# Kernel tuning notes

Hardware: AMD Instinct MI355X
Metric: run time of the kernel (lower is better)

The kernel has to match this reference:

```python
import jax, jax.numpy as jnp
import numpy as np
import math

B, S, D, H = 4, 2048, 1024, 16
DH = D // H  # per-head dim = 64
MASK_VAL = -1000000.0


def setup_inputs() -> dict:
    key = jax.random.key(0)
    ks = jax.random.split(key, 9)
    queries = jax.random.normal(ks[0], (B, S, D), dtype=jnp.float32)
    keys = jax.random.normal(ks[1], (B, S, D), dtype=jnp.float32)
    values = jax.random.normal(ks[2], (B, S, D), dtype=jnp.float32)
    valid_lens = jax.random.randint(ks[3], (B,), 0, S, dtype=jnp.int32)
    scale = 1.0 / math.sqrt(D)
    Wq = jax.random.normal(ks[4], (D, D), dtype=jnp.float32) * scale
    Wk = jax.random.normal(ks[5], (D, D), dtype=jnp.float32) * scale
    Wv = jax.random.normal(ks[6], (D, D), dtype=jnp.float32) * scale
    Wo = jax.random.normal(ks[7], (D, D), dtype=jnp.float32) * scale
    return {"queries": queries, "keys": keys, "values": values,
            "valid_lens": valid_lens, "Wq": Wq, "Wk": Wk, "Wv": Wv, "Wo": Wo}


def _split_heads(x):  # [B,S,D] -> [B,H,S,DH]
    b, s, _ = x.shape
    return x.reshape(b, s, H, DH).transpose(0, 2, 1, 3)


def reference(queries, keys, values, valid_lens, Wq, Wk, Wv, Wo):
    q = _split_heads(queries @ Wq)  # [B,H,S,DH]
    k = _split_heads(keys @ Wk)
    v = _split_heads(values @ Wv)
    scores = jnp.einsum('bhqd,bhkd->bhqk', q, k) / jnp.sqrt(jnp.float32(DH))
    # mask key positions >= valid_len[b] (sequence_mask with value=-1e6)
    key_pos = jnp.arange(S)  # [S]
    mask = key_pos[None, None, None, :] < valid_lens[:, None, None, None]  # [B,1,1,S]
    scores = jnp.where(mask, scores, MASK_VAL)
    attn = jax.nn.softmax(scores, axis=-1)  # [B,H,S,S] -- the 1GB intermediate
    out = jnp.einsum('bhqk,bhkd->bhqd', attn, v)  # [B,H,S,DH]
    out = out.transpose(0, 2, 1, 3).reshape(B, S, D)  # concat heads
    return out @ Wo
```

## Files before the change

### kernel.cpp

```cpp
#include <hip/hip_runtime.h>

#define BB 4
#define SS 2048
#define DD 1024
#define HH 16
#define DHH 64

typedef _Float16 half8 __attribute__((ext_vector_type(8)));
typedef _Float16 half4v __attribute__((ext_vector_type(4)));
typedef float floatx4 __attribute__((ext_vector_type(4)));

#define GLOBAL_AS __attribute__((address_space(1)))
#define LDS_AS __attribute__((address_space(3)))

__global__ void prep_kernel(const float* __restrict__ q, const float* __restrict__ k,
                            const float* __restrict__ v, const float* __restrict__ wq,
                            const float* __restrict__ wk, const float* __restrict__ wv,
                            const float* __restrict__ wo, _Float16* __restrict__ wt,
                            _Float16* __restrict__ acat, float* __restrict__ dout) {
  int bx = blockIdx.x;
  if (bx < 4096) {
    __shared__ float tile[32][33];
    int z = bx >> 10, rem = bx & 1023;
    const float* w = (z == 0) ? wq : (z == 1) ? wk : (z == 2) ? wv : wo;
    float scale = (z == 0) ? 0.125f : 1.0f;
    _Float16* dst = wt + (size_t)z * 1048576;
    int k0 = (rem >> 5) * 32, n0 = (rem & 31) * 32;
    int tx = threadIdx.x & 31, ty = threadIdx.x >> 5;
#pragma unroll
    for (int r = ty; r < 32; r += 8) tile[r][tx] = w[(size_t)(k0 + r) * 1024 + n0 + tx];
    __syncthreads();
#pragma unroll
    for (int r = ty; r < 32; r += 8)
      dst[(size_t)(n0 + r) * 1024 + k0 + tx] = (_Float16)(tile[tx][r] * scale);
  } else if (bx < 16384) {
    int idx = bx - 4096;
    int z = idx >> 12, xx = idx & 4095;
    const float* src = (z == 0) ? q : (z == 1) ? k : v;
    size_t i = ((size_t)xx * 256 + threadIdx.x) * 8;
    float4 f0 = *(const float4*)(src + i);
    float4 f1 = *(const float4*)(src + i + 4);
    half8 h = {(_Float16)f0.x, (_Float16)f0.y, (_Float16)f0.z, (_Float16)f0.w,
               (_Float16)f1.x, (_Float16)f1.y, (_Float16)f1.z, (_Float16)f1.w};
    *(half8*)(acat + (size_t)z * 8388608 + i) = h;
  } else {
    int idx = bx - 16384;
    size_t i = ((size_t)idx * 256 + threadIdx.x) * 8;
    float4 zz = {0.f, 0.f, 0.f, 0.f};
    *(float4*)(dout + i) = zz;
    *(float4*)(dout + i + 4) = zz;
  }
}

__global__ __launch_bounds__(256) void qkv_gemm(const _Float16* __restrict__ Acat,
                                                const _Float16* __restrict__ Wt,
                                                _Float16* __restrict__ Qf,
                                                _Float16* __restrict__ Kf,
                                                _Float16* __restrict__ Vt) {
  __shared__ _Float16 lA[128 * 32];
  __shared__ _Float16 lB[128 * 32];
  int tid = threadIdx.x;
  int wave = tid >> 6, lane = tid & 63, quad = lane >> 4, l15 = lane & 15;
  int bn = blockIdx.x, bm = blockIdx.y;
  int proj = bm >> 6;
  int wm = wave >> 1, wn = wave & 1;

  const _Float16* A = Acat + (size_t)bm * 128 * 1024;
  const _Float16* W = Wt + (size_t)proj * 1024 * 1024;

  floatx4 fzero = {0.f, 0.f, 0.f, 0.f};
  floatx4 acc[4][4];
#pragma unroll
  for (int i = 0; i < 4; ++i)
#pragma unroll
    for (int j = 0; j < 4; ++j) acc[i][j] = fzero;

  int g0 = tid, g1 = 256 + tid;
  int row0 = g0 >> 2, gc0 = (g0 & 3) ^ ((row0 >> 1) & 3);
  int row1 = g1 >> 2, gc1 = (g1 & 3) ^ ((row1 >> 1) & 3);
  const _Float16* a0 = A + ((size_t)row0 * 1024 + gc0 * 8);
  const _Float16* a1 = A + ((size_t)row1 * 1024 + gc1 * 8);
  const _Float16* b0 = W + ((size_t)(bn * 128 + row0) * 1024 + gc0 * 8);
  const _Float16* b1 = W + ((size_t)(bn * 128 + row1) * 1024 + gc1 * 8);

  for (int k0 = 0; k0 < 1024; k0 += 32) {
    __builtin_amdgcn_global_load_lds((const GLOBAL_AS void*)(a0 + k0),
                                     (LDS_AS void*)(lA + g0 * 8), 16, 0, 0);
    __builtin_amdgcn_global_load_lds((const GLOBAL_AS void*)(a1 + k0),
                                     (LDS_AS void*)(lA + g1 * 8), 16, 0, 0);
    __builtin_amdgcn_global_load_lds((const GLOBAL_AS void*)(b0 + k0),
                                     (LDS_AS void*)(lB + g0 * 8), 16, 0, 0);
    __builtin_amdgcn_global_load_lds((const GLOBAL_AS void*)(b1 + k0),
                                     (LDS_AS void*)(lB + g1 * 8), 16, 0, 0);
    __syncthreads();

    half8 af[4], bf[4];
#pragma unroll
    for (int i = 0; i < 4; ++i) {
      int row = wm * 64 + i * 16 + l15;
      af[i] = *(const half8*)(lA + (row * 4 + (quad ^ ((row >> 1) & 3))) * 8);
    }
#pragma unroll
    for (int j = 0; j < 4; ++j) {
      int row = wn * 64 + j * 16 + l15;
      bf[j] = *(const half8*)(lB + (row * 4 + (quad ^ ((row >> 1) & 3))) * 8);
    }
#pragma unroll
    for (int i = 0; i < 4; ++i)
#pragma unroll
      for (int j = 0; j < 4; ++j)
        acc[i][j] = __builtin_amdgcn_mfma_f32_16x16x32_f16(af[i], bf[j], acc[i][j], 0, 0, 0);
    __syncthreads();
  }

  int rloc = (bm & 63) * 128;
#pragma unroll
  for (int i = 0; i < 4; ++i) {
#pragma unroll
    for (int j = 0; j < 4; ++j) {
      int rowb = rloc + wm * 64 + i * 16 + quad * 4;
      int col = bn * 128 + wn * 64 + j * 16 + l15;
      if (proj < 2) {
        _Float16* dst = (proj == 0) ? Qf : Kf;
#pragma unroll
        for (int r = 0; r < 4; ++r)
          dst[(size_t)(rowb + r) * 1024 + col] = (_Float16)acc[i][j][r];
      } else {
        int b = rowb >> 11, s = rowb & 2047;
        half4v pk = {(_Float16)acc[i][j][0], (_Float16)acc[i][j][1],
                     (_Float16)acc[i][j][2], (_Float16)acc[i][j][3]};
        *(half4v*)(Vt + (size_t)(b * 1024 + col) * 2048 + s) = pk;
      }
    }
  }
}

__global__ __launch_bounds__(256) void gemm_out(const _Float16* __restrict__ A,
                                                const _Float16* __restrict__ Wt,
                                                float* __restrict__ C) {
  __shared__ _Float16 lA[128 * 32];
  __shared__ _Float16 lB[128 * 32];
  int tid = threadIdx.x;
  int wave = tid >> 6, lane = tid & 63, quad = lane >> 4, l15 = lane & 15;
  int bn = blockIdx.x, bm = blockIdx.y, kz = blockIdx.z;
  int wm = wave >> 1, wn = wave & 1;

  floatx4 fzero = {0.f, 0.f, 0.f, 0.f};
  floatx4 acc[4][4];
#pragma unroll
  for (int i = 0; i < 4; ++i)
#pragma unroll
    for (int j = 0; j < 4; ++j) acc[i][j] = fzero;

  int g0 = tid, g1 = 256 + tid;
  int row0 = g0 >> 2, gc0 = (g0 & 3) ^ ((row0 >> 1) & 3);
  int row1 = g1 >> 2, gc1 = (g1 & 3) ^ ((row1 >> 1) & 3);
  const _Float16* a0 = A + ((size_t)(bm * 128 + row0) * 1024 + gc0 * 8);
  const _Float16* a1 = A + ((size_t)(bm * 128 + row1) * 1024 + gc1 * 8);
  const _Float16* b0 = Wt + ((size_t)(bn * 128 + row0) * 1024 + gc0 * 8);
  const _Float16* b1 = Wt + ((size_t)(bn * 128 + row1) * 1024 + gc1 * 8);

  int kbeg = kz * 512, kend = kbeg + 512;
  for (int k0 = kbeg; k0 < kend; k0 += 32) {
    __builtin_amdgcn_global_load_lds((const GLOBAL_AS void*)(a0 + k0),
                                     (LDS_AS void*)(lA + g0 * 8), 16, 0, 0);
    __builtin_amdgcn_global_load_lds((const GLOBAL_AS void*)(a1 + k0),
                                     (LDS_AS void*)(lA + g1 * 8), 16, 0, 0);
    __builtin_amdgcn_global_load_lds((const GLOBAL_AS void*)(b0 + k0),
                                     (LDS_AS void*)(lB + g0 * 8), 16, 0, 0);
    __builtin_amdgcn_global_load_lds((const GLOBAL_AS void*)(b1 + k0),
                                     (LDS_AS void*)(lB + g1 * 8), 16, 0, 0);
    __syncthreads();

    half8 af[4], bf[4];
#pragma unroll
    for (int i = 0; i < 4; ++i) {
      int row = wm * 64 + i * 16 + l15;
      af[i] = *(const half8*)(lA + (row * 4 + (quad ^ ((row >> 1) & 3))) * 8);
    }
#pragma unroll
    for (int j = 0; j < 4; ++j) {
      int row = wn * 64 + j * 16 + l15;
      bf[j] = *(const half8*)(lB + (row * 4 + (quad ^ ((row >> 1) & 3))) * 8);
    }
#pragma unroll
    for (int i = 0; i < 4; ++i)
#pragma unroll
      for (int j = 0; j < 4; ++j)
        acc[i][j] = __builtin_amdgcn_mfma_f32_16x16x32_f16(af[i], bf[j], acc[i][j], 0, 0, 0);
    __syncthreads();
  }

#pragma unroll
  for (int i = 0; i < 4; ++i)
#pragma unroll
    for (int j = 0; j < 4; ++j) {
      int rowb = bm * 128 + wm * 64 + i * 16 + quad * 4;
      int col = bn * 128 + wn * 64 + j * 16 + l15;
#pragma unroll
      for (int r = 0; r < 4; ++r)
        atomicAdd(&C[(size_t)(rowb + r) * 1024 + col], acc[i][j][r]);
    }
}

__global__ __launch_bounds__(256) void attn_kernel(const _Float16* __restrict__ Q,
                                                   const _Float16* __restrict__ K,
                                                   const _Float16* __restrict__ Vt,
                                                   const int* __restrict__ vlens,
                                                   _Float16* __restrict__ O) {
  __shared__ _Float16 lK[64 * 64];
  __shared__ _Float16 lV[64 * 64];
  __shared__ _Float16 lP[4 * 16 * 64];

  int tid = threadIdx.x, wave = tid >> 6, lane = tid & 63, quad = lane >> 4, l15 = lane & 15;
  int bh = blockIdx.y, b = bh >> 4, h = bh & 15;
  int q0 = blockIdx.x * 64;
  int vlen = vlens[b];
  int nch = (vlen == 0) ? (SS / 64) : ((vlen + 63) >> 6);
  float mask_val = (vlen == 0) ? 0.0f : -1.0e6f;

  const _Float16* qb = Q + ((size_t)(b * SS + q0 + wave * 16 + l15) * DD + h * 64 + quad * 8);
  half8 qf0 = *(const half8*)qb;
  half8 qf1 = *(const half8*)(qb + 32);

  float l_part[4] = {0.f, 0.f, 0.f, 0.f};
  floatx4 fzero = {0.f, 0.f, 0.f, 0.f};
  floatx4 o[4];
#pragma unroll
  for (int j = 0; j < 4; ++j) o[j] = fzero;

  for (int kc = 0; kc < nch; ++kc) {
    int kb = kc * 64;
#pragma unroll
    for (int ss = tid; ss < 512; ss += 256) {
      int row = ss >> 3, gc = ss & 7;
      int sidx = (row * 8 + (gc ^ (row & 7))) * 8;
      *(half8*)(lK + sidx) =
          *(const half8*)(K + ((size_t)(b * SS + kb + row) * DD + h * 64 + gc * 8));
      *(half8*)(lV + sidx) =
          *(const half8*)(Vt + ((size_t)(b * DD + h * 64 + row) * SS + kb + gc * 8));
    }
    __syncthreads();

    floatx4 sacc[4];
#pragma unroll
    for (int j = 0; j < 4; ++j) sacc[j] = fzero;
#pragma unroll
    for (int ks = 0; ks < 2; ++ks) {
      half8 qf = ks ? qf1 : qf0;
#pragma unroll
      for (int j = 0; j < 4; ++j) {
        int row = j * 16 + l15, gc = ks * 4 + quad;
        half8 kf = *(const half8*)(lK + (row * 8 + (gc ^ (row & 7))) * 8);
        sacc[j] = __builtin_amdgcn_mfma_f32_16x16x32_f16(qf, kf, sacc[j], 0, 0, 0);
      }
    }

    bool clean = (kb + 64 <= vlen);
#pragma unroll
    for (int j = 0; j < 4; ++j) {
      int key = kb + j * 16 + l15;
      bool valid = clean | (key < vlen);
#pragma unroll
      for (int r = 0; r < 4; ++r) {
        float s = valid ? sacc[j][r] : mask_val;
        float p = __expf(s);
        l_part[r] += p;
        int row = quad * 4 + r, col = j * 16 + l15;
        int gc = col >> 3, off = col & 7;
        lP[wave * 1024 + row * 64 + (gc ^ (row & 7)) * 8 + off] = (_Float16)p;
      }
    }

#pragma unroll
    for (int ks = 0; ks < 2; ++ks) {
      int gc = ks * 4 + quad;
      half8 pf = *(const half8*)(lP + wave * 1024 + l15 * 64 + (gc ^ (l15 & 7)) * 8);
#pragma unroll
      for (int j = 0; j < 4; ++j) {
        int row = j * 16 + l15;
        half8 vf = *(const half8*)(lV + (row * 8 + (gc ^ (row & 7))) * 8);
        o[j] = __builtin_amdgcn_mfma_f32_16x16x32_f16(pf, vf, o[j], 0, 0, 0);
      }
    }
    __syncthreads();
  }

  float inv_l[4];
#pragma unroll
  for (int r = 0; r < 4; ++r) {
    float l = l_part[r];
#pragma unroll
    for (int off = 1; off < 16; off <<= 1) l += __shfl_xor(l, off);
    inv_l[r] = 1.0f / l;
  }
#pragma unroll
  for (int j = 0; j < 4; ++j) {
    int col = h * 64 + j * 16 + l15;
#pragma unroll
    for (int r = 0; r < 4; ++r) {
      int qrow = q0 + wave * 16 + quad * 4 + r;
      O[(size_t)(b * SS + qrow) * DD + col] = (_Float16)(o[j][r] * inv_l[r]);
    }
  }
}

extern "C" void kernel_launch(void* const* d_in, const int* in_sizes, int n_in,
                              void* d_out, int out_size, void* d_ws, size_t ws_size,
                              hipStream_t stream) {
  const float* q = (const float*)d_in[0];
  const float* k = (const float*)d_in[1];
  const float* v = (const float*)d_in[2];
  const int* vl = (const int*)d_in[3];
  const float* wq = (const float*)d_in[4];
  const float* wk = (const float*)d_in[5];
  const float* wv = (const float*)d_in[6];
  const float* wo = (const float*)d_in[7];

  char* ws = (char*)d_ws;
  _Float16* Wt = (_Float16*)ws;
  _Float16* Acat = (_Float16*)(ws + (8u << 20));
  _Float16* Qf = (_Float16*)(ws + (56u << 20));
  _Float16* Kf = (_Float16*)(ws + (72u << 20));
  _Float16* Vt = (_Float16*)(ws + (88u << 20));
  _Float16* Of = Acat;

  dim3 blk(256);

  prep_kernel<<<dim3(20480), blk, 0, stream>>>(q, k, v, wq, wk, wv, wo, Wt, Acat,
                                               (float*)d_out);
  qkv_gemm<<<dim3(8, 192), blk, 0, stream>>>(Acat, Wt, Qf, Kf, Vt);
  attn_kernel<<<dim3(32, 64), blk, 0, stream>>>(Qf, Kf, Vt, vl, Of);
  gemm_out<<<dim3(8, 64, 2), blk, 0, stream>>>(Of, Wt + 3 * 1048576, (float*)d_out);
}
```

Measured before the change: 384.5 us.

## Drop split-K atomics in output GEMM, async LDS loads and batch-interleaved grid in attention

The output projection no longer splits K across two blocks with atomicAdd into a zeroed buffer. Each block now covers the full K range and stores its results directly, which removes the zero-fill pass in prep_kernel and the atomic traffic, at the cost of half as many blocks. The attention kernel now stages K and V tiles into LDS with global_load_lds instead of register round-trips, hoisting the address setup out of the loop. Its grid is reordered so adjacent blocks cover different batches, mixing short and long valid lengths across CUs to even out load.

Measured after the change: 359.2 us. 6.6% less time.

```diff
diff --git a/kernel.cpp b/kernel.cpp
--- a/kernel.cpp
+++ b/kernel.cpp
@@ -17,7 +17,7 @@
                             const float* __restrict__ v, const float* __restrict__ wq,
                             const float* __restrict__ wk, const float* __restrict__ wv,
                             const float* __restrict__ wo, _Float16* __restrict__ wt,
-                            _Float16* __restrict__ acat, float* __restrict__ dout) {
+                            _Float16* __restrict__ acat) {
   int bx = blockIdx.x;
   if (bx < 4096) {
     __shared__ float tile[32][33];
@@ -33,7 +33,7 @@
 #pragma unroll
     for (int r = ty; r < 32; r += 8)
       dst[(size_t)(n0 + r) * 1024 + k0 + tx] = (_Float16)(tile[tx][r] * scale);
-  } else if (bx < 16384) {
+  } else {
     int idx = bx - 4096;
     int z = idx >> 12, xx = idx & 4095;
     const float* src = (z == 0) ? q : (z == 1) ? k : v;
@@ -43,12 +43,6 @@
     half8 h = {(_Float16)f0.x, (_Float16)f0.y, (_Float16)f0.z, (_Float16)f0.w,
                (_Float16)f1.x, (_Float16)f1.y, (_Float16)f1.z, (_Float16)f1.w};
     *(half8*)(acat + (size_t)z * 8388608 + i) = h;
-  } else {
-    int idx = bx - 16384;
-    size_t i = ((size_t)idx * 256 + threadIdx.x) * 8;
-    float4 zz = {0.f, 0.f, 0.f, 0.f};
-    *(float4*)(dout + i) = zz;
-    *(float4*)(dout + i + 4) = zz;
   }
 }
 
@@ -142,7 +136,7 @@
   __shared__ _Float16 lB[128 * 32];
   int tid = threadIdx.x;
   int wave = tid >> 6, lane = tid & 63, quad = lane >> 4, l15 = lane & 15;
-  int bn = blockIdx.x, bm = blockIdx.y, kz = blockIdx.z;
+  int bn = blockIdx.x, bm = blockIdx.y;
   int wm = wave >> 1, wn = wave & 1;
 
   floatx4 fzero = {0.f, 0.f, 0.f, 0.f};
@@ -160,8 +154,7 @@
   const _Float16* b0 = Wt + ((size_t)(bn * 128 + row0) * 1024 + gc0 * 8);
   const _Float16* b1 = Wt + ((size_t)(bn * 128 + row1) * 1024 + gc1 * 8);
 
-  int kbeg = kz * 512, kend = kbeg + 512;
-  for (int k0 = kbeg; k0 < kend; k0 += 32) {
+  for (int k0 = 0; k0 < 1024; k0 += 32) {
     __builtin_amdgcn_global_load_lds((const GLOBAL_AS void*)(a0 + k0),
                                      (LDS_AS void*)(lA + g0 * 8), 16, 0, 0);
     __builtin_amdgcn_global_load_lds((const GLOBAL_AS void*)(a1 + k0),
@@ -198,8 +191,7 @@
       int rowb = bm * 128 + wm * 64 + i * 16 + quad * 4;
       int col = bn * 128 + wn * 64 + j * 16 + l15;
 #pragma unroll
-      for (int r = 0; r < 4; ++r)
-        atomicAdd(&C[(size_t)(rowb + r) * 1024 + col], acc[i][j][r]);
+      for (int r = 0; r < 4; ++r) C[(size_t)(rowb + r) * 1024 + col] = acc[i][j][r];
     }
 }
 
@@ -213,8 +205,9 @@
   __shared__ _Float16 lP[4 * 16 * 64];
 
   int tid = threadIdx.x, wave = tid >> 6, lane = tid & 63, quad = lane >> 4, l15 = lane & 15;
-  int bh = blockIdx.y, b = bh >> 4, h = bh & 15;
-  int q0 = blockIdx.x * 64;
+  int bx = blockIdx.x;
+  int b = bx & 3, h = blockIdx.y;
+  int q0 = (bx >> 2) * 64;
   int vlen = vlens[b];
   int nch = (vlen == 0) ? (SS / 64) : ((vlen + 63) >> 6);
   float mask_val = (vlen == 0) ? 0.0f : -1.0e6f;
@@ -223,6 +216,14 @@
   half8 qf0 = *(const half8*)qb;
   half8 qf1 = *(const half8*)(qb + 32);
 
+  int g0 = tid, g1 = tid + 256;
+  int kr0 = g0 >> 3, kc0 = (g0 & 7) ^ (kr0 & 7);
+  int kr1 = g1 >> 3, kc1 = (g1 & 7) ^ (kr1 & 7);
+  const _Float16* ksrc0 = K + ((size_t)(b * SS + kr0) * DD + h * 64 + kc0 * 8);
+  const _Float16* ksrc1 = K + ((size_t)(b * SS + kr1) * DD + h * 64 + kc1 * 8);
+  const _Float16* vsrc0 = Vt + ((size_t)(b * DD + h * 64 + kr0) * SS + kc0 * 8);
+  const _Float16* vsrc1 = Vt + ((size_t)(b * DD + h * 64 + kr1) * SS + kc1 * 8);
+
   float l_part[4] = {0.f, 0.f, 0.f, 0.f};
   floatx4 fzero = {0.f, 0.f, 0.f, 0.f};
   floatx4 o[4];
@@ -231,15 +232,14 @@
 
   for (int kc = 0; kc < nch; ++kc) {
     int kb = kc * 64;
-#pragma unroll
-    for (int ss = tid; ss < 512; ss += 256) {
-      int row = ss >> 3, gc = ss & 7;
-      int sidx = (row * 8 + (gc ^ (row & 7))) * 8;
-      *(half8*)(lK + sidx) =
-          *(const half8*)(K + ((size_t)(b * SS + kb + row) * DD + h * 64 + gc * 8));
-      *(half8*)(lV + sidx) =
-          *(const half8*)(Vt + ((size_t)(b * DD + h * 64 + row) * SS + kb + gc * 8));
-    }
+    __builtin_amdgcn_global_load_lds((const GLOBAL_AS void*)(ksrc0 + (size_t)kb * DD),
+                                     (LDS_AS void*)(lK + g0 * 8), 16, 0, 0);
+    __builtin_amdgcn_global_load_lds((const GLOBAL_AS void*)(ksrc1 + (size_t)kb * DD),
+                                     (LDS_AS void*)(lK + g1 * 8), 16, 0, 0);
+    __builtin_amdgcn_global_load_lds((const GLOBAL_AS void*)(vsrc0 + kb),
+                                     (LDS_AS void*)(lV + g0 * 8), 16, 0, 0);
+    __builtin_amdgcn_global_load_lds((const GLOBAL_AS void*)(vsrc1 + kb),
+                                     (LDS_AS void*)(lV + g1 * 8), 16, 0, 0);
     __syncthreads();
 
     floatx4 sacc[4];
@@ -327,9 +327,8 @@
 
   dim3 blk(256);
 
-  prep_kernel<<<dim3(20480), blk, 0, stream>>>(q, k, v, wq, wk, wv, wo, Wt, Acat,
-                                               (float*)d_out);
+  prep_kernel<<<dim3(16384), blk, 0, stream>>>(q, k, v, wq, wk, wv, wo, Wt, Acat);
   qkv_gemm<<<dim3(8, 192), blk, 0, stream>>>(Acat, Wt, Qf, Kf, Vt);
-  attn_kernel<<<dim3(32, 64), blk, 0, stream>>>(Qf, Kf, Vt, vl, Of);
-  gemm_out<<<dim3(8, 64, 2), blk, 0, stream>>>(Of, Wt + 3 * 1048576, (float*)d_out);
-}
+  attn_kernel<<<dim3(128, 16), blk, 0, stream>>>(Qf, Kf, Vt, vl, Of);
+  gemm_out<<<dim3(8, 64), blk, 0, stream>>>(Of, Wt + 3 * 1048576, (float*)d_out);
+}
```
